# Performance work log

Hardware: AMD Instinct MI355X
Metric: run time of the kernel (lower is better)

The kernel has to match this reference:

```python
import jax, jax.numpy as jnp
import numpy as np

B, N, D, F, NRBF, H = 8, 256, 3, 32, 50, 128
EPS = 1e-6

# Levi-Civita tensor [3,3,3]
LC = jnp.array(np.array([[[0, 0, 0], [0, 0, 1], [0, -1, 0]],
                         [[0, 0, -1], [0, 0, 0], [1, 0, 0]],
                         [[0, 1, 0], [-1, 0, 0], [0, 0, 0]]], dtype=np.float32))

# off-diagonal neighbor indices: OFFD[i] = all j != i  -> [N, N-1]
OFFD = np.stack([np.concatenate([np.arange(i), np.arange(i + 1, N)]) for i in range(N)])


def mlp(x, W1, b1, W2, b2):
    return jax.nn.silu(x @ W1 + b1) @ W2 + b2


def rbf_encode(d, mus, gamma):
    # d: [B,N,N-1,1] -> [B,N,N-1,NRBF]
    return jnp.exp(-gamma * (d - mus) ** 2)


def setup_inputs() -> dict:
    key = jax.random.key(0)
    ks = jax.random.split(key, 8)
    p = lambda k, shape: 0.1 * jax.random.normal(k, shape, dtype=jnp.float32)
    IN = NRBF + 2 * F    # 114: rbfs + self feats + 'other' feats
    INF = NRBF + F       # 82: rbfs + softmax feats
    return {
        't': jnp.zeros((1,), jnp.float32),
        'state': jax.random.normal(ks[0], (B, N * D + N * F), dtype=jnp.float32),
        'mus': jnp.linspace(0.0, 5.0, NRBF, dtype=jnp.float32),
        'gamma': jnp.float32(10.0),
        's1_W1': p(ks[1], (IN, H)), 's1_b1': jnp.zeros((H,), jnp.float32),
        's1_W2': p(ks[2], (H, 1)), 's1_b2': jnp.zeros((1,), jnp.float32),
        's2_W1': p(ks[3], (IN, H)), 's2_b1': jnp.zeros((H,), jnp.float32),
        's2_W2': p(ks[4], (H, 1)), 's2_b2': jnp.zeros((1,), jnp.float32),
        'f_W1': p(ks[5], (INF, H)), 'f_b1': jnp.zeros((H,), jnp.float32),
        'f_W2': p(ks[6], (H, F)), 'f_b2': jnp.zeros((F,), jnp.float32),
    }


def reference(t, state, mus, gamma,
              s1_W1, s1_b1, s1_W2, s1_b2,
              s2_W1, s2_b1, s2_W2, s2_b2,
              f_W1, f_b1, f_W2, f_b2):
    x = state[:, :N * D].reshape(B, N, D)
    feats = state[:, N * D:].reshape(B, N, F)

    # distance vectors r[b,i,k] = x[b,i] - x[b, OFFD[i,k]]  -> [B,N,N-1,D]
    r = x[:, :, None, :] - x[:, OFFD, :]
    d = jnp.sqrt(jnp.sum(r ** 2, -1, keepdims=True) + EPS)  # [B,N,N-1,1]

    # NOTE: the torch tile+transpose+diagonal_filter yields other_feats[b,i,k] = feats[b,i]
    # (self features broadcast over neighbors); reproduced faithfully.
    feats_i = jnp.broadcast_to(feats[:, :, None, :], (B, N, N - 1, F))
    other_feats = feats_i

    rbfs = rbf_encode(d, mus, gamma)  # [B,N,N-1,NRBF]
    inp = jnp.concatenate([rbfs, feats_i, other_feats], -1)  # [B,N,N-1,114]

    # exact trace: grad of s1 wrt d contracted with r2d (torch.autograd.grad equivalent)
    def s1_of_d(dd):
        rb = rbf_encode(dd, mus, gamma)
        return mlp(jnp.concatenate([rb, feats_i, other_feats], -1), s1_W1, s1_b1, s1_W2, s1_b2)

    s1, vjp_fn = jax.vjp(s1_of_d, d)  # s1: [B,N,N-1,1]
    r2d = jnp.sum(r ** 2, -1, keepdims=True) / d
    (gd,) = vjp_fn(r2d)
    first_sum = jnp.sum(gd, axis=(1, 2))          # [B,1]
    second_sum = jnp.sum(s1 * D, axis=(1, 2))     # [B,1]
    trace = (first_sum + second_sum) / (N - 1)    # [B,1]

    s2 = mlp(inp, s2_W1, s2_b1, s2_W2, s2_b2)     # [B,N,N-1,1]

    # feature dynamics: cat(rbfs, softmax(other_feats)) -> MLP -> mean over neighbors
    inp_f = jnp.concatenate([rbfs, jax.nn.softmax(other_feats, axis=-1)], -1)
    v_feats = mlp(inp_f, f_W1, f_b1, f_W2, f_b2).mean(axis=2).reshape(B, N * F)

    v_x = (r * s1).mean(axis=2)  # [B,N,D]
    rr = jnp.einsum('ofi,nabf,nai->nabo', LC, r, v_x)  # [B,N,N-1,D]
    v_x = v_x + (rr * s2).mean(axis=2)
    v_x = (v_x - v_x.mean(axis=1, keepdims=True)).reshape(B, N * D)  # remove_mean

    v = jnp.concatenate([v_x, v_feats], axis=-1)  # [B, N*D + N*F]
    return v, trace
```

## Files before the change

### kernel.cpp

```cpp
#include <hip/hip_runtime.h>
#include <math.h>

#define Bn 8
#define Nn 256
#define Fn 32
#define NRBF 50
#define Hn 128
#define NK 255
#define ROW 8960
#define EPSf 1e-6f
#define KP 64
#define ASTR 72
#define L2E 1.44269504f

typedef __attribute__((ext_vector_type(8))) __bf16 b8;
typedef __attribute__((ext_vector_type(4))) float f32x4;

__device__ __forceinline__ float fast_sig(float z) {
    return __builtin_amdgcn_rcpf(1.f + __builtin_amdgcn_exp2f(-z * L2E));
}

__global__ __launch_bounds__(256) void pack_w_kernel(
    const float* __restrict__ s1_W1, const float* __restrict__ s2_W1,
    const float* __restrict__ f_W1,  const float* __restrict__ mus,
    __bf16* __restrict__ Wb)
{
    int idx = blockIdx.x * 256 + threadIdx.x;
    if (idx >= 4 * Hn * KP) return;
    int g = idx >> 13;
    int h = (idx >> 6) & 127;
    int k = idx & 63;
    float v = 0.f;
    if (k < NRBF) {
        if (g == 0)      v = s1_W1[k * Hn + h];
        else if (g == 1) v = s1_W1[k * Hn + h] * mus[k];
        else if (g == 2) v = s2_W1[k * Hn + h];
        else             v = f_W1[k * Hn + h];
    }
    Wb[idx] = (__bf16)v;
}

__global__ __launch_bounds__(256, 2) void pair_kernel(
    const float* __restrict__ state,
    const float* __restrict__ mus,   const float* __restrict__ gammap,
    const float* __restrict__ s1_W1, const float* __restrict__ s1_b1,
    const float* __restrict__ s1_W2, const float* __restrict__ s1_b2,
    const float* __restrict__ s2_W1, const float* __restrict__ s2_b1,
    const float* __restrict__ s2_W2, const float* __restrict__ s2_b2,
    const float* __restrict__ f_W1,  const float* __restrict__ f_b1,
    const float* __restrict__ f_W2,  const float* __restrict__ f_b2,
    const __bf16* __restrict__ Wb,
    float* __restrict__ vx_pre, float* __restrict__ tr_part,
    float* __restrict__ out)
{
    const int i = blockIdx.x, b = blockIdx.y;
    const int tid  = threadIdx.x;
    const int w    = tid >> 6;
    const int lane = tid & 63;
    const int c    = lane & 15;
    const int q    = lane >> 4;

    __shared__ __attribute__((aligned(16))) __bf16 As[256 * ASTR];
    __shared__ float xpos[Nn * 3];
    __shared__ float musS[NRBF];
    __shared__ float ff[Fn], sf[Fn];
    __shared__ float zf1s[Hn], zf2s[Hn], zffs[Hn];
    __shared__ float sW2a[Hn], sW2b[Hn];
    __shared__ float dsh[256];
    __shared__ float rsh[256][4];
    __shared__ float afsumsh[Hn];
    __shared__ float accum7[8];

    for (int t = tid; t < Nn * 3; t += 256) xpos[t] = state[b * ROW + t];
    if (tid < Fn)   ff[tid] = state[b * ROW + Nn * 3 + i * Fn + tid];
    if (tid < NRBF) musS[tid] = mus[tid];
    if (tid < Hn) { sW2a[tid] = s1_W2[tid]; sW2b[tid] = s2_W2[tid]; afsumsh[tid] = 0.f; }
    if (tid < 8)    accum7[tid] = 0.f;
    __syncthreads();

    const float gamma = gammap[0];

    if (tid < Fn) {
        float mx = -1e30f;
        for (int f = 0; f < Fn; f++) mx = fmaxf(mx, ff[f]);
        sf[tid] = __builtin_amdgcn_exp2f((ff[tid] - mx) * L2E);
    }

    {
        const float valid = (tid < NK) ? 1.f : 0.f;
        const int   kk    = (tid < NK) ? tid : 0;
        const int   j     = kk + (kk >= i ? 1 : 0);
        float rx = (xpos[i * 3 + 0] - xpos[j * 3 + 0]) * valid;
        float ry = (xpos[i * 3 + 1] - xpos[j * 3 + 1]) * valid;
        float rz = (xpos[i * 3 + 2] - xpos[j * 3 + 2]) * valid;
        float ssq = rx * rx + ry * ry + rz * rz;
        float dd  = sqrtf(ssq + EPSf);
        dsh[tid] = dd;
        rsh[tid][0] = rx; rsh[tid][1] = ry; rsh[tid][2] = rz; rsh[tid][3] = ssq;
        const float ngl = -gamma * L2E;
        #pragma unroll
        for (int ch = 0; ch < 8; ch++) {
            b8 v;
            #pragma unroll
            for (int jj = 0; jj < 8; jj++) {
                int m = ch * 8 + jj;
                float rv = 0.f;
                if (m < NRBF) {
                    float t = dd - musS[m];
                    rv = __builtin_amdgcn_exp2f(ngl * t * t) * valid;
                }
                v[jj] = (__bf16)rv;
            }
            *(b8*)&As[tid * ASTR + ch * 8] = v;
        }
    }
    __syncthreads();

    float ssum = 0.f;
    if (tid < Fn) { for (int f = 0; f < Fn; f++) ssum += sf[f]; }
    __syncthreads();
    if (tid < Fn) sf[tid] = sf[tid] * __builtin_amdgcn_rcpf(ssum);
    __syncthreads();

    if (tid < Hn) {
        int h = tid;
        float z1 = s1_b1[h], z2 = s2_b1[h], zf = f_b1[h];
        for (int f = 0; f < Fn; f++) {
            float fv = ff[f];
            z1 += fv * (s1_W1[(NRBF + f) * Hn + h] + s1_W1[(NRBF + Fn + f) * Hn + h]);
            z2 += fv * (s2_W1[(NRBF + f) * Hn + h] + s2_W1[(NRBF + Fn + f) * Hn + h]);
            zf += sf[f] * f_W1[(NRBF + f) * Hn + h];
        }
        zf1s[h] = z1; zf2s[h] = z2; zffs[h] = zf;
    }
    __syncthreads();

    b8 a0[4], a1[4];
    #pragma unroll
    for (int mc = 0; mc < 4; mc++) {
        const b8* Ar = (const b8*)&As[(w * 64 + mc * 16 + c) * ASTR];
        a0[mc] = Ar[q];
        a1[mc] = Ar[4 + q];
    }

    float dreg[16];
    #pragma unroll
    for (int mc = 0; mc < 4; mc++)
        #pragma unroll
        for (int r = 0; r < 4; r++)
            dreg[mc * 4 + r] = dsh[w * 64 + mc * 16 + q * 4 + r];

    float s1p[16], ds1p[16], s2p[16];
    #pragma unroll
    for (int t = 0; t < 16; t++) { s1p[t] = 0.f; ds1p[t] = 0.f; s2p[t] = 0.f; }

    for (int nt = 0; nt < 8; nt++) {
        int h = nt * 16 + c;
        const b8* B0 = (const b8*)&Wb[(0 * Hn + h) * KP];
        const b8* B1 = (const b8*)&Wb[(1 * Hn + h) * KP];
        b8 b00 = B0[q], b01 = B0[4 + q];
        b8 b10 = B1[q], b11 = B1[4 + q];
        float w2  = sW2a[h];
        float zf1 = zf1s[h];
        #pragma unroll
        for (int mc = 0; mc < 4; mc++) {
            f32x4 acc1 = {0.f, 0.f, 0.f, 0.f}, accm = {0.f, 0.f, 0.f, 0.f};
            acc1 = __builtin_amdgcn_mfma_f32_16x16x32_bf16(a0[mc], b00, acc1, 0, 0, 0);
            acc1 = __builtin_amdgcn_mfma_f32_16x16x32_bf16(a1[mc], b01, acc1, 0, 0, 0);
            accm = __builtin_amdgcn_mfma_f32_16x16x32_bf16(a0[mc], b10, accm, 0, 0, 0);
            accm = __builtin_amdgcn_mfma_f32_16x16x32_bf16(a1[mc], b11, accm, 0, 0, 0);
            #pragma unroll
            for (int r = 0; r < 4; r++) {
                int idx = mc * 4 + r;
                float zr1 = acc1[r];
                float z1  = zr1 + zf1;
                float sig = fast_sig(z1);
                s1p[idx]  = fmaf(z1 * sig, w2, s1p[idx]);
                float sp  = sig * fmaf(z1, 1.f - sig, 1.f);
                float t   = fmaf(dreg[idx], zr1, -accm[r]);
                ds1p[idx] = fmaf(w2 * sp, t, ds1p[idx]);
            }
        }
    }

    for (int nt = 0; nt < 8; nt++) {
        int h = nt * 16 + c;
        const b8* B2 = (const b8*)&Wb[(2 * Hn + h) * KP];
        b8 b20 = B2[q], b21 = B2[4 + q];
        float w2  = sW2b[h];
        float zf2 = zf2s[h];
        #pragma unroll
        for (int mc = 0; mc < 4; mc++) {
            f32x4 acc = {0.f, 0.f, 0.f, 0.f};
            acc = __builtin_amdgcn_mfma_f32_16x16x32_bf16(a0[mc], b20, acc, 0, 0, 0);
            acc = __builtin_amdgcn_mfma_f32_16x16x32_bf16(a1[mc], b21, acc, 0, 0, 0);
            #pragma unroll
            for (int r = 0; r < 4; r++) {
                int idx = mc * 4 + r;
                float z2  = acc[r] + zf2;
                float sig = fast_sig(z2);
                s2p[idx]  = fmaf(z2 * sig, w2, s2p[idx]);
            }
        }
    }

    for (int nt = 0; nt < 8; nt++) {
        int h = nt * 16 + c;
        const b8* B3 = (const b8*)&Wb[(3 * Hn + h) * KP];
        b8 b30 = B3[q], b31 = B3[4 + q];
        float zff = zffs[h];
        float afp = 0.f;
        #pragma unroll
        for (int mc = 0; mc < 4; mc++) {
            f32x4 acc = {0.f, 0.f, 0.f, 0.f};
            acc = __builtin_amdgcn_mfma_f32_16x16x32_bf16(a0[mc], b30, acc, 0, 0, 0);
            acc = __builtin_amdgcn_mfma_f32_16x16x32_bf16(a1[mc], b31, acc, 0, 0, 0);
            #pragma unroll
            for (int r = 0; r < 4; r++) {
                int row = w * 64 + mc * 16 + q * 4 + r;
                float z   = acc[r] + zff;
                float av  = z * fast_sig(z);
                afp += (row < NK) ? av : 0.f;
            }
        }
        afp += __shfl_xor(afp, 16, 64);
        afp += __shfl_xor(afp, 32, 64);
        if (lane < 16) atomicAdd(&afsumsh[h], afp);
    }

    #pragma unroll
    for (int off = 1; off < 16; off <<= 1) {
        #pragma unroll
        for (int t = 0; t < 16; t++) {
            s1p[t]  += __shfl_xor(s1p[t],  off, 64);
            ds1p[t] += __shfl_xor(ds1p[t], off, 64);
            s2p[t]  += __shfl_xor(s2p[t],  off, 64);
        }
    }

    if (c == 0) {
        const float b2_1 = s1_b2[0], b2_2 = s2_b2[0];
        const float n2g  = -2.f * gamma;
        float p0 = 0.f, p1 = 0.f, p2 = 0.f, p3 = 0.f, p4 = 0.f, p5 = 0.f, p6 = 0.f;
        #pragma unroll
        for (int mc = 0; mc < 4; mc++)
            #pragma unroll
            for (int r = 0; r < 4; r++) {
                int idx = mc * 4 + r;
                int row = w * 64 + mc * 16 + q * 4 + r;
                if (row < NK) {
                    float s1  = s1p[idx] + b2_1;
                    float s2v = s2p[idx] + b2_2;
                    float gd  = ds1p[idx] * n2g * rsh[row][3] * __builtin_amdgcn_rcpf(dreg[idx]);
                    float rx = rsh[row][0], ry = rsh[row][1], rz = rsh[row][2];
                    p0 += rx * s1;  p1 += ry * s1;  p2 += rz * s1;
                    p3 += rx * s2v; p4 += ry * s2v; p5 += rz * s2v;
                    p6 += gd + 3.f * s1;
                }
            }
        atomicAdd(&accum7[0], p0); atomicAdd(&accum7[1], p1);
        atomicAdd(&accum7[2], p2); atomicAdd(&accum7[3], p3);
        atomicAdd(&accum7[4], p4); atomicAdd(&accum7[5], p5);
        atomicAdd(&accum7[6], p6);
    }
    __syncthreads();

    if (tid == 0) {
        const float inv = 1.f / 255.f;
        float vx0 = accum7[0] * inv, vx1 = accum7[1] * inv, vx2 = accum7[2] * inv;
        float cx = (accum7[4] * vx2 - accum7[5] * vx1) * inv;
        float cy = (accum7[5] * vx0 - accum7[3] * vx2) * inv;
        float cz = (accum7[3] * vx1 - accum7[4] * vx0) * inv;
        int bi = b * Nn + i;
        vx_pre[bi * 4 + 0] = vx0 + cx;
        vx_pre[bi * 4 + 1] = vx1 + cy;
        vx_pre[bi * 4 + 2] = vx2 + cz;
        tr_part[bi] = accum7[6];
    }

    if (tid < Fn) {
        float acc = 0.f;
        for (int h = 0; h < Hn; h++) acc = fmaf(afsumsh[h], f_W2[h * Fn + tid], acc);
        out[b * ROW + Nn * 3 + i * Fn + tid] = fmaf(acc, 1.f / 255.f, f_b2[tid]);
    }
}

__global__ __launch_bounds__(256) void finalize_kernel(
    const float* __restrict__ vx_pre, const float* __restrict__ tr_part,
    float* __restrict__ out)
{
    int b = blockIdx.x, tid = threadIdx.x;
    int bi = b * Nn + tid;
    float v0 = vx_pre[bi * 4 + 0];
    float v1 = vx_pre[bi * 4 + 1];
    float v2 = vx_pre[bi * 4 + 2];
    float tr = tr_part[bi];

    __shared__ float red[4][4];
    __shared__ float fin[4];
    float vals[4] = {v0, v1, v2, tr};
    #pragma unroll
    for (int cc = 0; cc < 4; cc++) {
        float v = vals[cc];
        #pragma unroll
        for (int off = 32; off; off >>= 1) v += __shfl_down(v, off, 64);
        if ((tid & 63) == 0) red[tid >> 6][cc] = v;
    }
    __syncthreads();
    if (tid < 4) fin[tid] = red[0][tid] + red[1][tid] + red[2][tid] + red[3][tid];
    __syncthreads();

    out[b * ROW + tid * 3 + 0] = v0 - fin[0] * (1.f / 256.f);
    out[b * ROW + tid * 3 + 1] = v1 - fin[1] * (1.f / 256.f);
    out[b * ROW + tid * 3 + 2] = v2 - fin[2] * (1.f / 256.f);
    if (tid == 0) out[Bn * ROW + b] = fin[3] * (1.f / 255.f);
}

extern "C" void kernel_launch(void* const* d_in, const int* in_sizes, int n_in,
                              void* d_out, int out_size, void* d_ws, size_t ws_size,
                              hipStream_t stream)
{
    const float* state = (const float*)d_in[1];
    const float* mus   = (const float*)d_in[2];
    const float* gam   = (const float*)d_in[3];
    const float* s1_W1 = (const float*)d_in[4];
    const float* s1_b1 = (const float*)d_in[5];
    const float* s1_W2 = (const float*)d_in[6];
    const float* s1_b2 = (const float*)d_in[7];
    const float* s2_W1 = (const float*)d_in[8];
    const float* s2_b1 = (const float*)d_in[9];
    const float* s2_W2 = (const float*)d_in[10];
    const float* s2_b2 = (const float*)d_in[11];
    const float* f_W1  = (const float*)d_in[12];
    const float* f_b1  = (const float*)d_in[13];
    const float* f_W2  = (const float*)d_in[14];
    const float* f_b2  = (const float*)d_in[15];

    __bf16* Wb     = (__bf16*)d_ws;
    float*  vx_pre = (float*)((char*)d_ws + 4 * Hn * KP * sizeof(__bf16));
    float*  tr_part = vx_pre + Bn * Nn * 4;
    float*  out    = (float*)d_out;

    pack_w_kernel<<<(4 * Hn * KP + 255) / 256, 256, 0, stream>>>(s1_W1, s2_W1, f_W1, mus, Wb);

    dim3 grid(Nn, Bn);
    pair_kernel<<<grid, 256, 0, stream>>>(state, mus, gam,
        s1_W1, s1_b1, s1_W2, s1_b2,
        s2_W1, s2_b1, s2_W2, s2_b2,
        f_W1, f_b1, f_W2, f_b2,
        Wb, vx_pre, tr_part, out);

    finalize_kernel<<<Bn, 256, 0, stream>>>(vx_pre, tr_part, out);
}
```

Measured before the change: 210.8 us.

## Precompute per-atom feature bias terms in prep kernel and raise pair kernel occupancy

Moves the per-atom softmax and feature-contribution matvecs (zf1/zf2/zff) out of the pair kernel into a new prep kernel fused with weight packing, writing them to workspace. The pair kernel then reloads the A fragments per phase instead of keeping them live, splits the derivative accumulator into two terms to shorten the hidden loop, replaces the 16-way cross-lane reductions of per-row partials with a final full-wave reduction, recomputes r from positions instead of storing it in shared memory, and uses an XOR-swizzled A layout with no padding. Launch bounds are raised to 4 blocks per SM to increase occupancy. This adds workspace traffic and an extra ALU/shuffle path, and register pressure may cause spills at the new bound.

```diff
diff --git a/kernel.cpp b/kernel.cpp
--- a/kernel.cpp
+++ b/kernel.cpp
@@ -10,7 +10,6 @@
 #define ROW 8960
 #define EPSf 1e-6f
 #define KP 64
-#define ASTR 72
 #define L2E 1.44269504f
 
 typedef __attribute__((ext_vector_type(8))) __bf16 b8;
@@ -20,71 +19,115 @@
     return __builtin_amdgcn_rcpf(1.f + __builtin_amdgcn_exp2f(-z * L2E));
 }
 
-__global__ __launch_bounds__(256) void pack_w_kernel(
-    const float* __restrict__ s1_W1, const float* __restrict__ s2_W1,
-    const float* __restrict__ f_W1,  const float* __restrict__ mus,
-    __bf16* __restrict__ Wb)
+__device__ __forceinline__ int aswz(int row, int ch) {
+    return row * KP + ((ch ^ (row & 7)) << 3);
+}
+
+__global__ __launch_bounds__(256) void prep_kernel(
+    const float* __restrict__ s1_W1, const float* __restrict__ s1_b1,
+    const float* __restrict__ s2_W1, const float* __restrict__ s2_b1,
+    const float* __restrict__ f_W1,  const float* __restrict__ f_b1,
+    const float* __restrict__ mus,   const float* __restrict__ state,
+    __bf16* __restrict__ Wb,
+    float* __restrict__ zb1, float* __restrict__ zb2, float* __restrict__ zb3)
 {
-    int idx = blockIdx.x * 256 + threadIdx.x;
-    if (idx >= 4 * Hn * KP) return;
-    int g = idx >> 13;
-    int h = (idx >> 6) & 127;
-    int k = idx & 63;
-    float v = 0.f;
-    if (k < NRBF) {
-        if (g == 0)      v = s1_W1[k * Hn + h];
-        else if (g == 1) v = s1_W1[k * Hn + h] * mus[k];
-        else if (g == 2) v = s2_W1[k * Hn + h];
-        else             v = f_W1[k * Hn + h];
-    }
-    Wb[idx] = (__bf16)v;
-}
-
-__global__ __launch_bounds__(256, 2) void pair_kernel(
+    const int tid = threadIdx.x;
+    if (blockIdx.x < 128) {
+        int idx = blockIdx.x * 256 + tid;
+        int g = idx >> 13;
+        int h = (idx >> 6) & 127;
+        int k = idx & 63;
+        float v = 0.f;
+        if (k < NRBF) {
+            if (g == 0)      v = s1_W1[k * Hn + h];
+            else if (g == 1) v = s1_W1[k * Hn + h] * mus[k];
+            else if (g == 2) v = s2_W1[k * Hn + h];
+            else             v = f_W1[k * Hn + h];
+        }
+        Wb[idx] = (__bf16)v;
+        return;
+    }
+
+    const int p = blockIdx.x - 128;
+    const int b = p >> 8, i = p & 255;
+
+    __shared__ float ff[Fn], sf[Fn];
+    if (tid < Fn) ff[tid] = state[b * ROW + Nn * 3 + i * Fn + tid];
+    __syncthreads();
+    if (tid < Fn) {
+        float mx = -1e30f;
+        for (int f = 0; f < Fn; f++) mx = fmaxf(mx, ff[f]);
+        sf[tid] = __builtin_amdgcn_exp2f((ff[tid] - mx) * L2E);
+    }
+    __syncthreads();
+    if (tid < Fn) {
+        float s = 0.f;
+        for (int f = 0; f < Fn; f++) s += sf[f];
+        sf[tid] = sf[tid] * __builtin_amdgcn_rcpf(s);
+    }
+    __syncthreads();
+
+    const int h = tid & 127;
+    if (tid < 128) {
+        float z1 = s1_b1[h], z2 = s2_b1[h];
+        for (int f = 0; f < Fn; f++) {
+            float fv = ff[f];
+            z1 += fv * (s1_W1[(NRBF + f) * Hn + h] + s1_W1[(NRBF + Fn + f) * Hn + h]);
+            z2 += fv * (s2_W1[(NRBF + f) * Hn + h] + s2_W1[(NRBF + Fn + f) * Hn + h]);
+        }
+        zb1[p * Hn + h] = z1;
+        zb2[p * Hn + h] = z2;
+    } else {
+        float zf = f_b1[h];
+        for (int f = 0; f < Fn; f++)
+            zf += sf[f] * f_W1[(NRBF + f) * Hn + h];
+        zb3[p * Hn + h] = zf;
+    }
+}
+
+__global__ __launch_bounds__(256, 4) void pair_kernel(
     const float* __restrict__ state,
     const float* __restrict__ mus,   const float* __restrict__ gammap,
-    const float* __restrict__ s1_W1, const float* __restrict__ s1_b1,
     const float* __restrict__ s1_W2, const float* __restrict__ s1_b2,
-    const float* __restrict__ s2_W1, const float* __restrict__ s2_b1,
     const float* __restrict__ s2_W2, const float* __restrict__ s2_b2,
-    const float* __restrict__ f_W1,  const float* __restrict__ f_b1,
     const float* __restrict__ f_W2,  const float* __restrict__ f_b2,
     const __bf16* __restrict__ Wb,
+    const float* __restrict__ zb1, const float* __restrict__ zb2,
+    const float* __restrict__ zb3,
     float* __restrict__ vx_pre, float* __restrict__ tr_part,
     float* __restrict__ out)
 {
     const int i = blockIdx.x, b = blockIdx.y;
+    const int pi = b * Nn + i;
     const int tid  = threadIdx.x;
     const int w    = tid >> 6;
     const int lane = tid & 63;
     const int c    = lane & 15;
     const int q    = lane >> 4;
 
-    __shared__ __attribute__((aligned(16))) __bf16 As[256 * ASTR];
+    __shared__ __attribute__((aligned(16))) __bf16 As[256 * KP];
     __shared__ float xpos[Nn * 3];
-    __shared__ float musS[NRBF];
-    __shared__ float ff[Fn], sf[Fn];
+    __shared__ float dsh[256];
+    __shared__ float musS[52];
     __shared__ float zf1s[Hn], zf2s[Hn], zffs[Hn];
     __shared__ float sW2a[Hn], sW2b[Hn];
-    __shared__ float dsh[256];
-    __shared__ float rsh[256][4];
     __shared__ float afsumsh[Hn];
     __shared__ float accum7[8];
 
     for (int t = tid; t < Nn * 3; t += 256) xpos[t] = state[b * ROW + t];
-    if (tid < Fn)   ff[tid] = state[b * ROW + Nn * 3 + i * Fn + tid];
     if (tid < NRBF) musS[tid] = mus[tid];
-    if (tid < Hn) { sW2a[tid] = s1_W2[tid]; sW2b[tid] = s2_W2[tid]; afsumsh[tid] = 0.f; }
-    if (tid < 8)    accum7[tid] = 0.f;
+    if (tid < Hn) {
+        zf1s[tid] = zb1[pi * Hn + tid];
+        zf2s[tid] = zb2[pi * Hn + tid];
+        zffs[tid] = zb3[pi * Hn + tid];
+        sW2a[tid] = s1_W2[tid];
+        sW2b[tid] = s2_W2[tid];
+        afsumsh[tid] = 0.f;
+    }
+    if (tid < 8) accum7[tid] = 0.f;
     __syncthreads();
 
     const float gamma = gammap[0];
-
-    if (tid < Fn) {
-        float mx = -1e30f;
-        for (int f = 0; f < Fn; f++) mx = fmaxf(mx, ff[f]);
-        sf[tid] = __builtin_amdgcn_exp2f((ff[tid] - mx) * L2E);
-    }
 
     {
         const float valid = (tid < NK) ? 1.f : 0.f;
@@ -96,7 +139,6 @@
         float ssq = rx * rx + ry * ry + rz * rz;
         float dd  = sqrtf(ssq + EPSf);
         dsh[tid] = dd;
-        rsh[tid][0] = rx; rsh[tid][1] = ry; rsh[tid][2] = rz; rsh[tid][3] = ssq;
         const float ngl = -gamma * L2E;
         #pragma unroll
         for (int ch = 0; ch < 8; ch++) {
@@ -111,157 +153,154 @@
                 }
                 v[jj] = (__bf16)rv;
             }
-            *(b8*)&As[tid * ASTR + ch * 8] = v;
-        }
-    }
-    __syncthreads();
-
-    float ssum = 0.f;
-    if (tid < Fn) { for (int f = 0; f < Fn; f++) ssum += sf[f]; }
-    __syncthreads();
-    if (tid < Fn) sf[tid] = sf[tid] * __builtin_amdgcn_rcpf(ssum);
-    __syncthreads();
-
-    if (tid < Hn) {
-        int h = tid;
-        float z1 = s1_b1[h], z2 = s2_b1[h], zf = f_b1[h];
-        for (int f = 0; f < Fn; f++) {
-            float fv = ff[f];
-            z1 += fv * (s1_W1[(NRBF + f) * Hn + h] + s1_W1[(NRBF + Fn + f) * Hn + h]);
-            z2 += fv * (s2_W1[(NRBF + f) * Hn + h] + s2_W1[(NRBF + Fn + f) * Hn + h]);
-            zf += sf[f] * f_W1[(NRBF + f) * Hn + h];
-        }
-        zf1s[h] = z1; zf2s[h] = z2; zffs[h] = zf;
-    }
-    __syncthreads();
-
-    b8 a0[4], a1[4];
+            *(b8*)&As[aswz(tid, ch)] = v;
+        }
+    }
+    __syncthreads();
+
+    const int row0 = w * 64;
+
+    float s1p[16], ds1a[16], ds1b[16], s2p[16];
     #pragma unroll
-    for (int mc = 0; mc < 4; mc++) {
-        const b8* Ar = (const b8*)&As[(w * 64 + mc * 16 + c) * ASTR];
-        a0[mc] = Ar[q];
-        a1[mc] = Ar[4 + q];
-    }
-
-    float dreg[16];
-    #pragma unroll
-    for (int mc = 0; mc < 4; mc++)
-        #pragma unroll
-        for (int r = 0; r < 4; r++)
-            dreg[mc * 4 + r] = dsh[w * 64 + mc * 16 + q * 4 + r];
-
-    float s1p[16], ds1p[16], s2p[16];
-    #pragma unroll
-    for (int t = 0; t < 16; t++) { s1p[t] = 0.f; ds1p[t] = 0.f; s2p[t] = 0.f; }
-
-    for (int nt = 0; nt < 8; nt++) {
-        int h = nt * 16 + c;
-        const b8* B0 = (const b8*)&Wb[(0 * Hn + h) * KP];
-        const b8* B1 = (const b8*)&Wb[(1 * Hn + h) * KP];
-        b8 b00 = B0[q], b01 = B0[4 + q];
-        b8 b10 = B1[q], b11 = B1[4 + q];
-        float w2  = sW2a[h];
-        float zf1 = zf1s[h];
+    for (int t = 0; t < 16; t++) { s1p[t] = 0.f; ds1a[t] = 0.f; ds1b[t] = 0.f; s2p[t] = 0.f; }
+
+    {
+        b8 a0[4], a1[4];
         #pragma unroll
         for (int mc = 0; mc < 4; mc++) {
-            f32x4 acc1 = {0.f, 0.f, 0.f, 0.f}, accm = {0.f, 0.f, 0.f, 0.f};
-            acc1 = __builtin_amdgcn_mfma_f32_16x16x32_bf16(a0[mc], b00, acc1, 0, 0, 0);
-            acc1 = __builtin_amdgcn_mfma_f32_16x16x32_bf16(a1[mc], b01, acc1, 0, 0, 0);
-            accm = __builtin_amdgcn_mfma_f32_16x16x32_bf16(a0[mc], b10, accm, 0, 0, 0);
-            accm = __builtin_amdgcn_mfma_f32_16x16x32_bf16(a1[mc], b11, accm, 0, 0, 0);
+            int rrow = row0 + mc * 16 + c;
+            a0[mc] = *(const b8*)&As[aswz(rrow, q)];
+            a1[mc] = *(const b8*)&As[aswz(rrow, 4 + q)];
+        }
+        for (int nt = 0; nt < 8; nt++) {
+            int h = nt * 16 + c;
+            const b8* B0 = (const b8*)&Wb[(0 * Hn + h) * KP];
+            const b8* B1 = (const b8*)&Wb[(1 * Hn + h) * KP];
+            b8 b00 = B0[q], b01 = B0[4 + q];
+            b8 b10 = B1[q], b11 = B1[4 + q];
+            float w2  = sW2a[h];
+            float zf1 = zf1s[h];
+            #pragma unroll
+            for (int mc = 0; mc < 4; mc++) {
+                f32x4 acc1 = {0.f, 0.f, 0.f, 0.f}, accm = {0.f, 0.f, 0.f, 0.f};
+                acc1 = __builtin_amdgcn_mfma_f32_16x16x32_bf16(a0[mc], b00, acc1, 0, 0, 0);
+                acc1 = __builtin_amdgcn_mfma_f32_16x16x32_bf16(a1[mc], b01, acc1, 0, 0, 0);
+                accm = __builtin_amdgcn_mfma_f32_16x16x32_bf16(a0[mc], b10, accm, 0, 0, 0);
+                accm = __builtin_amdgcn_mfma_f32_16x16x32_bf16(a1[mc], b11, accm, 0, 0, 0);
+                #pragma unroll
+                for (int r = 0; r < 4; r++) {
+                    int idx = mc * 4 + r;
+                    float zr1 = acc1[r];
+                    float z1  = zr1 + zf1;
+                    float sig = fast_sig(z1);
+                    s1p[idx]  = fmaf(z1 * sig, w2, s1p[idx]);
+                    float cc  = w2 * (sig * fmaf(z1, 1.f - sig, 1.f));
+                    ds1a[idx] = fmaf(cc, zr1, ds1a[idx]);
+                    ds1b[idx] = fmaf(cc, accm[r], ds1b[idx]);
+                }
+            }
+        }
+    }
+
+    {
+        b8 a0[4], a1[4];
+        #pragma unroll
+        for (int mc = 0; mc < 4; mc++) {
+            int rrow = row0 + mc * 16 + c;
+            a0[mc] = *(const b8*)&As[aswz(rrow, q)];
+            a1[mc] = *(const b8*)&As[aswz(rrow, 4 + q)];
+        }
+        for (int nt = 0; nt < 8; nt++) {
+            int h = nt * 16 + c;
+            const b8* B2 = (const b8*)&Wb[(2 * Hn + h) * KP];
+            b8 b20 = B2[q], b21 = B2[4 + q];
+            float w2  = sW2b[h];
+            float zf2 = zf2s[h];
+            #pragma unroll
+            for (int mc = 0; mc < 4; mc++) {
+                f32x4 acc = {0.f, 0.f, 0.f, 0.f};
+                acc = __builtin_amdgcn_mfma_f32_16x16x32_bf16(a0[mc], b20, acc, 0, 0, 0);
+                acc = __builtin_amdgcn_mfma_f32_16x16x32_bf16(a1[mc], b21, acc, 0, 0, 0);
+                #pragma unroll
+                for (int r = 0; r < 4; r++) {
+                    int idx = mc * 4 + r;
+                    float z2  = acc[r] + zf2;
+                    s2p[idx]  = fmaf(z2 * fast_sig(z2), w2, s2p[idx]);
+                }
+            }
+        }
+    }
+
+    {
+        const float b2_1 = (c == 0) ? s1_b2[0] : 0.f;
+        const float b2_2 = (c == 0) ? s2_b2[0] : 0.f;
+        const float n2g  = -2.f * gamma;
+        const float xi0 = xpos[i * 3 + 0], xi1 = xpos[i * 3 + 1], xi2 = xpos[i * 3 + 2];
+        float p0 = 0.f, p1 = 0.f, p2 = 0.f, p3 = 0.f, p4 = 0.f, p5 = 0.f, p6 = 0.f;
+        #pragma unroll
+        for (int mc = 0; mc < 4; mc++)
             #pragma unroll
             for (int r = 0; r < 4; r++) {
                 int idx = mc * 4 + r;
-                float zr1 = acc1[r];
-                float z1  = zr1 + zf1;
-                float sig = fast_sig(z1);
-                s1p[idx]  = fmaf(z1 * sig, w2, s1p[idx]);
-                float sp  = sig * fmaf(z1, 1.f - sig, 1.f);
-                float t   = fmaf(dreg[idx], zr1, -accm[r]);
-                ds1p[idx] = fmaf(w2 * sp, t, ds1p[idx]);
-            }
-        }
-    }
-
-    for (int nt = 0; nt < 8; nt++) {
-        int h = nt * 16 + c;
-        const b8* B2 = (const b8*)&Wb[(2 * Hn + h) * KP];
-        b8 b20 = B2[q], b21 = B2[4 + q];
-        float w2  = sW2b[h];
-        float zf2 = zf2s[h];
+                int row = row0 + mc * 16 + q * 4 + r;
+                if (row < NK) {
+                    int j = row + (row >= i ? 1 : 0);
+                    float rx = xi0 - xpos[j * 3 + 0];
+                    float ry = xi1 - xpos[j * 3 + 1];
+                    float rz = xi2 - xpos[j * 3 + 2];
+                    float ssq = rx * rx + ry * ry + rz * rz;
+                    float dd  = dsh[row];
+                    float e1  = s1p[idx] + b2_1;
+                    float e2  = s2p[idx] + b2_2;
+                    float e3  = fmaf(dd, ds1a[idx], -ds1b[idx]);
+                    float fr  = n2g * ssq * __builtin_amdgcn_rcpf(dd);
+                    p0 = fmaf(rx, e1, p0); p1 = fmaf(ry, e1, p1); p2 = fmaf(rz, e1, p2);
+                    p3 = fmaf(rx, e2, p3); p4 = fmaf(ry, e2, p4); p5 = fmaf(rz, e2, p5);
+                    p6 = fmaf(fr, e3, fmaf(3.f, e1, p6));
+                }
+            }
+        float ps[7] = {p0, p1, p2, p3, p4, p5, p6};
+        #pragma unroll
+        for (int off = 1; off < 64; off <<= 1)
+            #pragma unroll
+            for (int t = 0; t < 7; t++) ps[t] += __shfl_xor(ps[t], off, 64);
+        if (lane == 0) {
+            #pragma unroll
+            for (int t = 0; t < 7; t++) atomicAdd(&accum7[t], ps[t]);
+        }
+    }
+
+    {
+        b8 a0[4], a1[4];
         #pragma unroll
         for (int mc = 0; mc < 4; mc++) {
-            f32x4 acc = {0.f, 0.f, 0.f, 0.f};
-            acc = __builtin_amdgcn_mfma_f32_16x16x32_bf16(a0[mc], b20, acc, 0, 0, 0);
-            acc = __builtin_amdgcn_mfma_f32_16x16x32_bf16(a1[mc], b21, acc, 0, 0, 0);
-            #pragma unroll
-            for (int r = 0; r < 4; r++) {
-                int idx = mc * 4 + r;
-                float z2  = acc[r] + zf2;
-                float sig = fast_sig(z2);
-                s2p[idx]  = fmaf(z2 * sig, w2, s2p[idx]);
-            }
-        }
-    }
-
-    for (int nt = 0; nt < 8; nt++) {
-        int h = nt * 16 + c;
-        const b8* B3 = (const b8*)&Wb[(3 * Hn + h) * KP];
-        b8 b30 = B3[q], b31 = B3[4 + q];
-        float zff = zffs[h];
-        float afp = 0.f;
-        #pragma unroll
-        for (int mc = 0; mc < 4; mc++) {
-            f32x4 acc = {0.f, 0.f, 0.f, 0.f};
-            acc = __builtin_amdgcn_mfma_f32_16x16x32_bf16(a0[mc], b30, acc, 0, 0, 0);
-            acc = __builtin_amdgcn_mfma_f32_16x16x32_bf16(a1[mc], b31, acc, 0, 0, 0);
-            #pragma unroll
-            for (int r = 0; r < 4; r++) {
-                int row = w * 64 + mc * 16 + q * 4 + r;
-                float z   = acc[r] + zff;
-                float av  = z * fast_sig(z);
-                afp += (row < NK) ? av : 0.f;
-            }
-        }
-        afp += __shfl_xor(afp, 16, 64);
-        afp += __shfl_xor(afp, 32, 64);
-        if (lane < 16) atomicAdd(&afsumsh[h], afp);
-    }
-
-    #pragma unroll
-    for (int off = 1; off < 16; off <<= 1) {
-        #pragma unroll
-        for (int t = 0; t < 16; t++) {
-            s1p[t]  += __shfl_xor(s1p[t],  off, 64);
-            ds1p[t] += __shfl_xor(ds1p[t], off, 64);
-            s2p[t]  += __shfl_xor(s2p[t],  off, 64);
-        }
-    }
-
-    if (c == 0) {
-        const float b2_1 = s1_b2[0], b2_2 = s2_b2[0];
-        const float n2g  = -2.f * gamma;
-        float p0 = 0.f, p1 = 0.f, p2 = 0.f, p3 = 0.f, p4 = 0.f, p5 = 0.f, p6 = 0.f;
-        #pragma unroll
-        for (int mc = 0; mc < 4; mc++)
-            #pragma unroll
-            for (int r = 0; r < 4; r++) {
-                int idx = mc * 4 + r;
-                int row = w * 64 + mc * 16 + q * 4 + r;
-                if (row < NK) {
-                    float s1  = s1p[idx] + b2_1;
-                    float s2v = s2p[idx] + b2_2;
-                    float gd  = ds1p[idx] * n2g * rsh[row][3] * __builtin_amdgcn_rcpf(dreg[idx]);
-                    float rx = rsh[row][0], ry = rsh[row][1], rz = rsh[row][2];
-                    p0 += rx * s1;  p1 += ry * s1;  p2 += rz * s1;
-                    p3 += rx * s2v; p4 += ry * s2v; p5 += rz * s2v;
-                    p6 += gd + 3.f * s1;
-                }
-            }
-        atomicAdd(&accum7[0], p0); atomicAdd(&accum7[1], p1);
-        atomicAdd(&accum7[2], p2); atomicAdd(&accum7[3], p3);
-        atomicAdd(&accum7[4], p4); atomicAdd(&accum7[5], p5);
-        atomicAdd(&accum7[6], p6);
+            int rrow = row0 + mc * 16 + c;
+            a0[mc] = *(const b8*)&As[aswz(rrow, q)];
+            a1[mc] = *(const b8*)&As[aswz(rrow, 4 + q)];
+        }
+        for (int nt = 0; nt < 8; nt++) {
+            int h = nt * 16 + c;
+            const b8* B3 = (const b8*)&Wb[(3 * Hn + h) * KP];
+            b8 b30 = B3[q], b31 = B3[4 + q];
+            float zff = zffs[h];
+            float afp = 0.f;
+            #pragma unroll
+            for (int mc = 0; mc < 4; mc++) {
+                f32x4 acc = {0.f, 0.f, 0.f, 0.f};
+                acc = __builtin_amdgcn_mfma_f32_16x16x32_bf16(a0[mc], b30, acc, 0, 0, 0);
+                acc = __builtin_amdgcn_mfma_f32_16x16x32_bf16(a1[mc], b31, acc, 0, 0, 0);
+                #pragma unroll
+                for (int r = 0; r < 4; r++) {
+                    int row = row0 + mc * 16 + q * 4 + r;
+                    float z  = acc[r] + zff;
+                    float av = z * fast_sig(z);
+                    afp += (row < NK) ? av : 0.f;
+                }
+            }
+            afp += __shfl_xor(afp, 16, 64);
+            afp += __shfl_xor(afp, 32, 64);
+            if (lane < 16) atomicAdd(&afsumsh[h], afp);
+        }
     }
     __syncthreads();
 
@@ -271,11 +310,10 @@
         float cx = (accum7[4] * vx2 - accum7[5] * vx1) * inv;
         float cy = (accum7[5] * vx0 - accum7[3] * vx2) * inv;
         float cz = (accum7[3] * vx1 - accum7[4] * vx0) * inv;
-        int bi = b * Nn + i;
-        vx_pre[bi * 4 + 0] = vx0 + cx;
-        vx_pre[bi * 4 + 1] = vx1 + cy;
-        vx_pre[bi * 4 + 2] = vx2 + cz;
-        tr_part[bi] = accum7[6];
+        vx_pre[pi * 4 + 0] = vx0 + cx;
+        vx_pre[pi * 4 + 1] = vx1 + cy;
+        vx_pre[pi * 4 + 2] = vx2 + cz;
+        tr_part[pi] = accum7[6];
     }
 
     if (tid < Fn) {
@@ -336,19 +374,22 @@
     const float* f_W2  = (const float*)d_in[14];
     const float* f_b2  = (const float*)d_in[15];
 
-    __bf16* Wb     = (__bf16*)d_ws;
-    float*  vx_pre = (float*)((char*)d_ws + 4 * Hn * KP * sizeof(__bf16));
-    float*  tr_part = vx_pre + Bn * Nn * 4;
-    float*  out    = (float*)d_out;
-
-    pack_w_kernel<<<(4 * Hn * KP + 255) / 256, 256, 0, stream>>>(s1_W1, s2_W1, f_W1, mus, Wb);
+    char* wsb = (char*)d_ws;
+    __bf16* Wb   = (__bf16*)wsb;
+    float* zb1   = (float*)(wsb + 65536);
+    float* zb2   = zb1 + Bn * Nn * Hn;
+    float* zb3   = zb2 + Bn * Nn * Hn;
+    float* vx_pre  = zb3 + Bn * Nn * Hn;
+    float* tr_part = vx_pre + Bn * Nn * 4;
+    float* out   = (float*)d_out;
+
+    prep_kernel<<<128 + Bn * Nn, 256, 0, stream>>>(
+        s1_W1, s1_b1, s2_W1, s2_b1, f_W1, f_b1, mus, state, Wb, zb1, zb2, zb3);
 
     dim3 grid(Nn, Bn);
     pair_kernel<<<grid, 256, 0, stream>>>(state, mus, gam,
-        s1_W1, s1_b1, s1_W2, s1_b2,
-        s2_W1, s2_b1, s2_W2, s2_b2,
-        f_W1, f_b1, f_W2, f_b2,
-        Wb, vx_pre, tr_part, out);
+        s1_W2, s1_b2, s2_W2, s2_b2, f_W2, f_b2,
+        Wb, zb1, zb2, zb3, vx_pre, tr_part, out);
 
     finalize_kernel<<<Bn, 256, 0, stream>>>(vx_pre, tr_part, out);
 }
```

Measured after the change: 296.7 us. 40.8% more time.
